# Performance work log

Measured on AMD Instinct MI355X. Metric: run time of the kernel, lower is better.

## Reference

```python
import jax, jax.numpy as jnp
import numpy as np

HIDDEN = 768
HEADS = 12
HEAD_DIM = HIDDEN // HEADS


def setup_inputs() -> dict:
    key = jax.random.key(0)
    ks = jax.random.split(key, 9)
    B, S = 2, 2048
    scale = 1.0 / np.sqrt(HIDDEN)
    return {
        "hidden_states": jax.random.normal(ks[0], (B, S, HIDDEN), jnp.float32),
        "context": jax.random.normal(ks[1], (B, S, HIDDEN), jnp.float32),
        "attention_mask": jnp.zeros((B, 1, 1, S), jnp.float32),
        "Wq": jax.random.normal(ks[2], (HIDDEN, HIDDEN), jnp.float32) * scale,
        "bq": jnp.zeros((HIDDEN,), jnp.float32),
        "Wk": jax.random.normal(ks[3], (HIDDEN, HIDDEN), jnp.float32) * scale,
        "bk": jnp.zeros((HIDDEN,), jnp.float32),
        "Wv": jax.random.normal(ks[4], (HIDDEN, HIDDEN), jnp.float32) * scale,
        "bv": jnp.zeros((HIDDEN,), jnp.float32),
    }


def _split_heads(x):
    # [B, S, H*D] -> [B, H, S, D]
    B, S, _ = x.shape
    return x.reshape(B, S, HEADS, HEAD_DIM).transpose(0, 2, 1, 3)


def reference(hidden_states, context, attention_mask, Wq, bq, Wk, bk, Wv, bv):
    # torch Linear: y = x @ W^T + b
    q = _split_heads(hidden_states @ Wq.T + bq)   # [B,H,Sq,D]
    k = _split_heads(context @ Wk.T + bk)         # [B,H,Sk,D]
    v = _split_heads(context @ Wv.T + bv)         # [B,H,Sk,D]

    scores = jnp.einsum("bhqd,bhkd->bhqk", q, k)
    scores = scores / np.sqrt(HEAD_DIM + 1e-05)
    scores = scores + attention_mask
    probs = jax.nn.softmax(scores, axis=-1)       # dropout p=0 -> identity (eval)
    ctx = jnp.einsum("bhqk,bhkd->bhqd", probs, v) # [B,H,Sq,D]
    B, H, Sq, D = ctx.shape
    return ctx.transpose(0, 2, 1, 3).reshape(B, Sq, H * D)
```

## Files before the change

### kernel.cpp

```cpp
#include <hip/hip_runtime.h>
#include <hip/hip_bf16.h>
#include <math.h>

typedef short s16x8 __attribute__((ext_vector_type(8)));
typedef float f32x4 __attribute__((ext_vector_type(4)));
typedef _Float16 f16x4 __attribute__((ext_vector_type(4)));
typedef __fp16 fp16x2 __attribute__((ext_vector_type(2)));
typedef unsigned short u16;

#define NHEADS 12
#define SEQ 2048
#define NBH 24
#define KDIM 768
#define LOG2E 1.44269504088896f

#define SWZ(row, col) (((row) * 64) + ((col) ^ (((row) & 7) << 3)))
#define SWZ32(row, col) (((row) * 32) + ((col) ^ (((row) & 3) << 3)))

#define GLOAD_LDS16(g, l) __builtin_amdgcn_global_load_lds( \
    (const __attribute__((address_space(1))) unsigned int*)(g), \
    (__attribute__((address_space(3))) unsigned int*)(l), 16, 0, 0)

static __device__ __forceinline__ u16 f2bf(float f) {
    union { float f; unsigned u; } v; v.f = f;
    unsigned r = v.u + 0x7fffu + ((v.u >> 16) & 1u);
    return (u16)(r >> 16);
}
static __device__ __forceinline__ u16 f2h(float f) {
    union { _Float16 h; u16 u; } v; v.h = (_Float16)f;
    return v.u;
}
static __device__ __forceinline__ f16x4 pack4(float a, float b, float c, float d) {
    union { fp16x2 h2[2]; f16x4 h4; } u;
    u.h2[0] = __builtin_amdgcn_cvt_pkrtz(a, b);
    u.h2[1] = __builtin_amdgcn_cvt_pkrtz(c, d);
    return u.h4;
}

__global__ void cvt6_kernel(const float* __restrict__ s0, const float* __restrict__ s1,
                            const float* __restrict__ s2, const float* __restrict__ s3,
                            const float* __restrict__ s4, const float* __restrict__ s5,
                            u16* __restrict__ d0, u16* __restrict__ d1, u16* __restrict__ d2,
                            u16* __restrict__ d3, u16* __restrict__ d4, float* __restrict__ d5,
                            int n4a, int n4w, float qscl) {
    const int z = blockIdx.z;
    int i = blockIdx.x * blockDim.x + threadIdx.x;
    if (z == 5) {
        if (i < (2 * SEQ) / 4) {
            float4 f = ((const float4*)s5)[i];
            f.x *= LOG2E; f.y *= LOG2E; f.z *= LOG2E; f.w *= LOG2E;
            ((float4*)d5)[i] = f;
        }
        return;
    }
    const float* src = (z == 0) ? s0 : (z == 1) ? s1 : (z == 2) ? s2 : (z == 3) ? s3 : s4;
    u16* dst         = (z == 0) ? d0 : (z == 1) ? d1 : (z == 2) ? d2 : (z == 3) ? d3 : d4;
    const int n4     = (z < 2) ? n4a : n4w;
    const float scl  = (z == 2) ? qscl : 1.0f;
    if (i < n4) {
        float4 f = ((const float4*)src)[i];
        ushort4 o;
        o.x = f2bf(f.x * scl); o.y = f2bf(f.y * scl); o.z = f2bf(f.z * scl); o.w = f2bf(f.w * scl);
        ((ushort4*)dst)[i] = o;
    }
}

__launch_bounds__(256)
__global__ void qkv_gemm(const u16* __restrict__ X, const u16* __restrict__ C,
                         const u16* __restrict__ W0, const u16* __restrict__ W1, const u16* __restrict__ W2,
                         const float* __restrict__ b0, const float* __restrict__ b1, const float* __restrict__ b2,
                         u16* __restrict__ Qo, u16* __restrict__ Ko, u16* __restrict__ Vo, float qscl) {
    const int z = blockIdx.z;
    const u16* A    = (z == 0) ? X  : C;
    const u16* W    = (z == 0) ? W0 : (z == 1) ? W1 : W2;
    const float* bi = (z == 0) ? b0 : (z == 1) ? b1 : b2;
    u16* out        = (z == 0) ? Qo : (z == 1) ? Ko : Vo;
    const float bscl = (z == 0) ? qscl : 1.0f;

    __shared__ u16 As[2][128 * 32];
    __shared__ u16 Bs[2][128 * 32];

    const int tid  = threadIdx.x;
    const int lane = tid & 63;
    const int wid  = tid >> 6;
    const int wr = wid >> 1, wc = wid & 1;
    const int l15 = lane & 15, lh = lane >> 4;
    const int mBase = blockIdx.x * 128;
    const int nBase = blockIdx.y * 128;

    size_t aSrc[2], bSrc[2]; int ldsOffG[2];
    #pragma unroll
    for (int i = 0; i < 2; ++i) {
        int L = tid * 8 + i * 2048;
        int row = L >> 5;
        int col = (L & 31) ^ ((row & 3) << 3);
        aSrc[i] = (size_t)(mBase + row) * KDIM + col;
        bSrc[i] = (size_t)(nBase + row) * KDIM + col;
        ldsOffG[i] = wid * 512 + i * 2048;
    }

    f32x4 acc[4][4] = {};

    #pragma unroll
    for (int i = 0; i < 2; ++i) {
        GLOAD_LDS16(&A[aSrc[i]], &As[0][ldsOffG[i]]);
        GLOAD_LDS16(&W[bSrc[i]], &Bs[0][ldsOffG[i]]);
    }

    const int NIT = KDIM / 32;
    for (int it = 0; it < NIT; ++it) {
        const int cur = it & 1;
        __syncthreads();
        if (it + 1 < NIT) {
            const int kb = (it + 1) * 32;
            #pragma unroll
            for (int i = 0; i < 2; ++i) {
                GLOAD_LDS16(&A[aSrc[i] + kb], &As[cur ^ 1][ldsOffG[i]]);
                GLOAD_LDS16(&W[bSrc[i] + kb], &Bs[cur ^ 1][ldsOffG[i]]);
            }
        }
        s16x8 xf[4], wf[4];
        #pragma unroll
        for (int m = 0; m < 4; ++m)
            xf[m] = *(const s16x8*)(&As[cur][SWZ32(wr * 64 + m * 16 + l15, lh * 8)]);
        #pragma unroll
        for (int n = 0; n < 4; ++n)
            wf[n] = *(const s16x8*)(&Bs[cur][SWZ32(wc * 64 + n * 16 + l15, lh * 8)]);
        if (z < 2) {
            #pragma unroll
            for (int m = 0; m < 4; ++m)
                #pragma unroll
                for (int n = 0; n < 4; ++n)
                    acc[m][n] = __builtin_amdgcn_mfma_f32_16x16x32_bf16(wf[n], xf[m], acc[m][n], 0, 0, 0);
        } else {
            #pragma unroll
            for (int m = 0; m < 4; ++m)
                #pragma unroll
                for (int n = 0; n < 4; ++n)
                    acc[m][n] = __builtin_amdgcn_mfma_f32_16x16x32_bf16(xf[m], wf[n], acc[m][n], 0, 0, 0);
        }
    }

    if (z < 2) {
        #pragma unroll
        for (int m = 0; m < 4; ++m) {
            int sg = mBase + wr * 64 + m * 16 + l15;
            int b = sg >> 11, s = sg & 2047;
            #pragma unroll
            for (int n = 0; n < 4; ++n) {
                int d0 = nBase + wc * 64 + n * 16 + lh * 4;
                int h = d0 >> 6, d = d0 & 63;
                float4 bv = *(const float4*)(&bi[d0]);
                ushort4 o;
                o.x = f2bf(acc[m][n][0] + bv.x * bscl);
                o.y = f2bf(acc[m][n][1] + bv.y * bscl);
                o.z = f2bf(acc[m][n][2] + bv.z * bscl);
                o.w = f2bf(acc[m][n][3] + bv.w * bscl);
                *(ushort4*)(&out[(((size_t)(b * NHEADS + h) * SEQ + s) << 6) + d]) = o;
            }
        }
    } else {
        #pragma unroll
        for (int m = 0; m < 4; ++m) {
            #pragma unroll
            for (int n = 0; n < 4; ++n) {
                int colg = nBase + wc * 64 + n * 16 + l15;
                float bv = bi[colg];
                int h = colg >> 6, d = colg & 63;
                int rowg0 = mBase + wr * 64 + m * 16 + lh * 4;
                int b = rowg0 >> 11, s = rowg0 & 2047;
                int sp = (s & ~0x3C) | (((s >> 2) & 3) << 4) | (((s >> 4) & 3) << 2);
                ushort4 o;
                o.x = f2h(acc[m][n][0] + bv);
                o.y = f2h(acc[m][n][1] + bv);
                o.z = f2h(acc[m][n][2] + bv);
                o.w = f2h(acc[m][n][3] + bv);
                *(ushort4*)(&out[(((size_t)(b * NHEADS + h) * 64 + d) << 11) + sp]) = o;
            }
        }
    }
}

template<bool SPLIT>
__launch_bounds__(512)
__global__ void attn_kernel(const u16* __restrict__ Qg, const u16* __restrict__ Kg,
                            const u16* __restrict__ Vg,
                            const float* __restrict__ maskL, float* __restrict__ out,
                            u16* __restrict__ OpartH, float* __restrict__ MLpart) {
    __shared__ u16 Ks[2][64 * 64];
    __shared__ u16 Vt[2][64 * 64];
    __shared__ float maskLds[2048];

    const int tid  = threadIdx.x;
    const int lane = tid & 63;
    const int wid  = tid >> 6;
    const int bh = blockIdx.y;
    const int b = bh / NHEADS;
    const int h = bh % NHEADS;
    const int q0 = blockIdx.x * 128 + wid * 16;
    const int l15 = lane & 15, lh = lane >> 4;
    const int z = SPLIT ? blockIdx.z : 0;
    const int NT = SPLIT ? (SEQ / 128) : (SEQ / 64);
    const int tile0 = z * NT;

    for (int i = tid * 4; i < NT * 64; i += 512 * 4)
        *(float4*)(&maskLds[i]) = *(const float4*)(&maskL[(size_t)b * SEQ + (tile0 << 6) + i]);

    const int srow = tid >> 3;
    const int scol = ((tid & 7) * 8) ^ ((srow & 7) << 3);
    const size_t kSrc = (((size_t)bh * SEQ + srow) << 6) + scol + ((size_t)tile0 << 12);
    const size_t vSrc = (((size_t)bh * 64 + srow) << 11) + scol + (size_t)tile0 * 64;
    const int ldsBase = wid * 512;

    s16x8 qf[2];
    #pragma unroll
    for (int kk = 0; kk < 2; ++kk)
        qf[kk] = *(const s16x8*)(&Qg[(((size_t)bh * SEQ + q0 + l15) << 6) + kk * 32 + lh * 8]);

    f32x4 oacc[4] = {};
    float mrun = -1e30f, lrun = 0.f;

    GLOAD_LDS16(&Kg[kSrc], &Ks[0][ldsBase]);
    GLOAD_LDS16(&Vg[vSrc], &Vt[0][ldsBase]);

    for (int t = 0; t < NT; ++t) {
        const int cur = t & 1;
        __syncthreads();
        if (t + 1 < NT) {
            GLOAD_LDS16(&Kg[kSrc + ((size_t)(t + 1) << 12)], &Ks[cur ^ 1][ldsBase]);
            GLOAD_LDS16(&Vg[vSrc + (size_t)(t + 1) * 64],    &Vt[cur ^ 1][ldsBase]);
        }

        f32x4 sacc[4];
        #pragma unroll
        for (int n = 0; n < 4; ++n) {
            float4 mv = *(const float4*)(&maskLds[t * 64 + n * 16 + lh * 4]);
            sacc[n][0] = mv.x; sacc[n][1] = mv.y; sacc[n][2] = mv.z; sacc[n][3] = mv.w;
        }
        __builtin_amdgcn_s_setprio(1);
        #pragma unroll
        for (int kk = 0; kk < 2; ++kk) {
            #pragma unroll
            for (int n = 0; n < 4; ++n) {
                s16x8 kf = *(const s16x8*)(&Ks[cur][SWZ(n * 16 + l15, kk * 32 + lh * 8)]);
                sacc[n] = __builtin_amdgcn_mfma_f32_16x16x32_bf16(kf, qf[kk], sacc[n], 0, 0, 0);
            }
        }
        __builtin_amdgcn_s_setprio(0);

        float tmax = sacc[0][0];
        #pragma unroll
        for (int n = 0; n < 4; ++n)
            #pragma unroll
            for (int j = 0; j < 4; ++j)
                tmax = fmaxf(tmax, sacc[n][j]);

        if (!__all(tmax - mrun <= 11.0f)) {
            float rmax = fmaxf(tmax, __shfl_xor(tmax, 16));
            rmax = fmaxf(rmax, __shfl_xor(rmax, 32));
            float mnew = fmaxf(mrun, rmax);
            float alpha = __builtin_amdgcn_exp2f(mrun - mnew);
            lrun *= alpha;
            #pragma unroll
            for (int nd = 0; nd < 4; ++nd)
                #pragma unroll
                for (int j = 0; j < 4; ++j)
                    oacc[nd][j] *= alpha;
            mrun = mnew;
        }

        f16x4 pf[4];
        #pragma unroll
        for (int n = 0; n < 4; ++n) {
            float p0 = __builtin_amdgcn_exp2f(sacc[n][0] - mrun);
            float p1 = __builtin_amdgcn_exp2f(sacc[n][1] - mrun);
            float p2 = __builtin_amdgcn_exp2f(sacc[n][2] - mrun);
            float p3 = __builtin_amdgcn_exp2f(sacc[n][3] - mrun);
            lrun += (p0 + p1) + (p2 + p3);
            pf[n] = pack4(p0, p1, p2, p3);
        }

        __builtin_amdgcn_s_setprio(1);
        #pragma unroll
        for (int kk = 0; kk < 2; ++kk) {
            #pragma unroll
            for (int nd = 0; nd < 4; ++nd) {
                s16x8 v2 = *(const s16x8*)(&Vt[cur][SWZ(nd * 16 + l15, lh * 16 + kk * 8)]);
                union { s16x8 s8; f16x4 h4[2]; } u; u.s8 = v2;
                oacc[nd] = __builtin_amdgcn_mfma_f32_16x16x16f16(u.h4[0], pf[2 * kk],     oacc[nd], 0, 0, 0);
                oacc[nd] = __builtin_amdgcn_mfma_f32_16x16x16f16(u.h4[1], pf[2 * kk + 1], oacc[nd], 0, 0, 0);
            }
        }
        __builtin_amdgcn_s_setprio(0);
    }

    lrun += __shfl_xor(lrun, 16);
    lrun += __shfl_xor(lrun, 32);

    const float inv = 1.0f / lrun;
    const int s = q0 + l15;
    if (!SPLIT) {
        #pragma unroll
        for (int nd = 0; nd < 4; ++nd) {
            float4 o;
            o.x = oacc[nd][0] * inv; o.y = oacc[nd][1] * inv;
            o.z = oacc[nd][2] * inv; o.w = oacc[nd][3] * inv;
            *(float4*)(&out[(size_t)(b * SEQ + s) * (NHEADS * 64) + h * 64 + nd * 16 + lh * 4]) = o;
        }
    } else {
        const size_t rbase = ((size_t)(z * NBH + bh) * SEQ + s);
        #pragma unroll
        for (int nd = 0; nd < 4; ++nd) {
            union { f16x4 h4; ushort4 u4; } o;
            o.h4 = pack4(oacc[nd][0] * inv, oacc[nd][1] * inv,
                         oacc[nd][2] * inv, oacc[nd][3] * inv);
            *(ushort4*)(&OpartH[rbase * 64 + nd * 16 + lh * 4]) = o.u4;
        }
        if (lh == 0)
            *(float2*)(&MLpart[rbase * 2]) = make_float2(mrun, lrun);
    }
}

__global__ void combine_kernel(const u16* __restrict__ OpartH, const float* __restrict__ MLpart,
                               float* __restrict__ out) {
    int gid = blockIdx.x * 256 + threadIdx.x;
    int row = gid >> 4, d4 = gid & 15;
    float2 ml0 = ((const float2*)MLpart)[row];
    float2 ml1 = ((const float2*)MLpart)[NBH * SEQ + row];
    float m = fmaxf(ml0.x, ml1.x);
    float w0 = __builtin_amdgcn_exp2f(ml0.x - m) * ml0.y;
    float w1 = __builtin_amdgcn_exp2f(ml1.x - m) * ml1.y;
    float inv = 1.0f / (w0 + w1);
    w0 *= inv; w1 *= inv;
    union { ushort4 u4; f16x4 h4; } a, c;
    a.u4 = *(const ushort4*)(&OpartH[(size_t)row * 64 + d4 * 4]);
    c.u4 = *(const ushort4*)(&OpartH[(size_t)NBH * SEQ * 64 + (size_t)row * 64 + d4 * 4]);
    float4 o;
    o.x = (float)a.h4[0] * w0 + (float)c.h4[0] * w1;
    o.y = (float)a.h4[1] * w0 + (float)c.h4[1] * w1;
    o.z = (float)a.h4[2] * w0 + (float)c.h4[2] * w1;
    o.w = (float)a.h4[3] * w0 + (float)c.h4[3] * w1;
    int bh = row >> 11, s = row & 2047;
    int b = bh / NHEADS, hh = bh % NHEADS;
    *(float4*)(&out[(size_t)(b * SEQ + s) * (NHEADS * 64) + hh * 64 + d4 * 4]) = o;
}

extern "C" void kernel_launch(void* const* d_in, const int* in_sizes, int n_in,
                              void* d_out, int out_size, void* d_ws, size_t ws_size,
                              hipStream_t stream) {
    const float* hidden  = (const float*)d_in[0];
    const float* context = (const float*)d_in[1];
    const float* mask    = (const float*)d_in[2];
    const float* Wq = (const float*)d_in[3];
    const float* bq = (const float*)d_in[4];
    const float* Wk = (const float*)d_in[5];
    const float* bk = (const float*)d_in[6];
    const float* Wv = (const float*)d_in[7];
    const float* bv = (const float*)d_in[8];
    float* out = (float*)d_out;

    char* ws = (char*)d_ws;
    const size_t XSZ = (size_t)4096 * 768 * 2;
    const size_t WSZ = (size_t)768 * 768 * 2;
    u16* X16  = (u16*)(ws);
    u16* C16  = (u16*)(ws + XSZ);
    u16* W16q = (u16*)(ws + 2 * XSZ);
    u16* W16k = (u16*)(ws + 2 * XSZ + WSZ);
    u16* W16v = (u16*)(ws + 2 * XSZ + 2 * WSZ);
    u16* Q16  = (u16*)(ws + 2 * XSZ + 3 * WSZ);
    u16* K16  = (u16*)(ws + 3 * XSZ + 3 * WSZ);
    u16* V16  = (u16*)(ws + 4 * XSZ + 3 * WSZ);
    const size_t MASKL_OFF = 5 * XSZ + 3 * WSZ;
    float* maskL = (float*)(ws + MASKL_OFF);
    const size_t OPART_OFF = MASKL_OFF + 2 * SEQ * sizeof(float) + 256;
    u16* OpartH = (u16*)(ws + OPART_OFF);
    const size_t ML_OFF = OPART_OFF + (size_t)2 * NBH * SEQ * 64 * 2;
    float* MLpart = (float*)(ws + ML_OFF);
    const size_t WS_NEED_SPLIT = ML_OFF + (size_t)2 * NBH * SEQ * 2 * 4;

    const float qscl = (float)((1.0 / sqrt(64.0 + 1e-5)) * 1.44269504088896);

    const int n4x = 4096 * 768 / 4;
    const int n4w = 768 * 768 / 4;
    cvt6_kernel<<<dim3((n4x + 255) / 256, 1, 6), 256, 0, stream>>>(
        hidden, context, Wq, Wk, Wv, mask,
        X16, C16, W16q, W16k, W16v, maskL, n4x, n4w, qscl);

    qkv_gemm<<<dim3(4096 / 128, 768 / 128, 3), 256, 0, stream>>>(
        X16, C16, W16q, W16k, W16v, bq, bk, bv, Q16, K16, V16, qscl);

    if (ws_size >= WS_NEED_SPLIT) {
        attn_kernel<true><<<dim3(SEQ / 128, NBH, 2), 512, 0, stream>>>(
            Q16, K16, V16, maskL, out, OpartH, MLpart);
        combine_kernel<<<(NBH * SEQ * 16) / 256, 256, 0, stream>>>(OpartH, MLpart, out);
    } else {
        attn_kernel<false><<<dim3(SEQ / 128, NBH, 1), 512, 0, stream>>>(
            Q16, K16, V16, maskL, out, OpartH, MLpart);
    }
}
```

Baseline: 101.4 us.

## Triple-buffer QKV GEMM LDS with vmcnt waits and a pair-row swizzle

Moves the QKV projection GEMM from double to triple LDS buffering with a prefetch distance of two k-steps. A fine-grained s_waitcnt vmcnt plus a raw s_barrier replaces __syncthreads, and prefetches are issued after the MFMAs instead of before. It also changes the LDS layout so two 32-wide rows share one 64-wide row under the 8-way XOR swizzle, meant to reduce bank conflicts on fragment reads. The cost is 50% more LDS per block, which may lower occupancy, and it relies on hand-counted vmcnt values staying correct.

```diff
diff --git a/kernel.cpp b/kernel.cpp
--- a/kernel.cpp
+++ b/kernel.cpp
@@ -15,7 +15,6 @@
 #define LOG2E 1.44269504088896f
 
 #define SWZ(row, col) (((row) * 64) + ((col) ^ (((row) & 7) << 3)))
-#define SWZ32(row, col) (((row) * 32) + ((col) ^ (((row) & 3) << 3)))
 
 #define GLOAD_LDS16(g, l) __builtin_amdgcn_global_load_lds( \
     (const __attribute__((address_space(1))) unsigned int*)(g), \
@@ -77,8 +76,8 @@
     u16* out        = (z == 0) ? Qo : (z == 1) ? Ko : Vo;
     const float bscl = (z == 0) ? qscl : 1.0f;
 
-    __shared__ u16 As[2][128 * 32];
-    __shared__ u16 Bs[2][128 * 32];
+    __shared__ u16 As[3][4096];
+    __shared__ u16 Bs[3][4096];
 
     const int tid  = threadIdx.x;
     const int lane = tid & 63;
@@ -88,44 +87,51 @@
     const int mBase = blockIdx.x * 128;
     const int nBase = blockIdx.y * 128;
 
-    size_t aSrc[2], bSrc[2]; int ldsOffG[2];
+    size_t aSrc[2], bSrc[2]; int ldsOff[2];
     #pragma unroll
     for (int i = 0; i < 2; ++i) {
-        int L = tid * 8 + i * 2048;
-        int row = L >> 5;
-        int col = (L & 31) ^ ((row & 3) << 3);
+        int L = i * 2048 + tid * 8;
+        int prow = L >> 6;
+        int pcol = (L & 63) ^ ((prow & 7) << 3);
+        int row = (prow << 1) | (pcol >> 5);
+        int col = pcol & 31;
         aSrc[i] = (size_t)(mBase + row) * KDIM + col;
         bSrc[i] = (size_t)(nBase + row) * KDIM + col;
-        ldsOffG[i] = wid * 512 + i * 2048;
-    }
+        ldsOff[i] = i * 2048 + wid * 512;
+    }
+
+#define G_STAGE(step, buf) do { \
+        const size_t kb_ = (size_t)(step) * 32; \
+        GLOAD_LDS16(&A[aSrc[0] + kb_], &As[buf][ldsOff[0]]); \
+        GLOAD_LDS16(&A[aSrc[1] + kb_], &As[buf][ldsOff[1]]); \
+        GLOAD_LDS16(&W[bSrc[0] + kb_], &Bs[buf][ldsOff[0]]); \
+        GLOAD_LDS16(&W[bSrc[1] + kb_], &Bs[buf][ldsOff[1]]); \
+    } while (0)
 
     f32x4 acc[4][4] = {};
 
-    #pragma unroll
-    for (int i = 0; i < 2; ++i) {
-        GLOAD_LDS16(&A[aSrc[i]], &As[0][ldsOffG[i]]);
-        GLOAD_LDS16(&W[bSrc[i]], &Bs[0][ldsOffG[i]]);
-    }
+    G_STAGE(0, 0);
+    G_STAGE(1, 1);
 
     const int NIT = KDIM / 32;
+    int cur = 0;
     for (int it = 0; it < NIT; ++it) {
-        const int cur = it & 1;
-        __syncthreads();
-        if (it + 1 < NIT) {
-            const int kb = (it + 1) * 32;
-            #pragma unroll
-            for (int i = 0; i < 2; ++i) {
-                GLOAD_LDS16(&A[aSrc[i] + kb], &As[cur ^ 1][ldsOffG[i]]);
-                GLOAD_LDS16(&W[bSrc[i] + kb], &Bs[cur ^ 1][ldsOffG[i]]);
-            }
-        }
+        if (it + 1 < NIT) asm volatile("s_waitcnt vmcnt(4)" ::: "memory");
+        else              asm volatile("s_waitcnt vmcnt(0)" ::: "memory");
+        __builtin_amdgcn_s_barrier();
+        __builtin_amdgcn_sched_barrier(0);
+
         s16x8 xf[4], wf[4];
         #pragma unroll
-        for (int m = 0; m < 4; ++m)
-            xf[m] = *(const s16x8*)(&As[cur][SWZ32(wr * 64 + m * 16 + l15, lh * 8)]);
-        #pragma unroll
-        for (int n = 0; n < 4; ++n)
-            wf[n] = *(const s16x8*)(&Bs[cur][SWZ32(wc * 64 + n * 16 + l15, lh * 8)]);
+        for (int m = 0; m < 4; ++m) {
+            int row = wr * 64 + m * 16 + l15;
+            xf[m] = *(const s16x8*)(&As[cur][SWZ(row >> 1, (row & 1) * 32 + lh * 8)]);
+        }
+        #pragma unroll
+        for (int n = 0; n < 4; ++n) {
+            int row = wc * 64 + n * 16 + l15;
+            wf[n] = *(const s16x8*)(&Bs[cur][SWZ(row >> 1, (row & 1) * 32 + lh * 8)]);
+        }
         if (z < 2) {
             #pragma unroll
             for (int m = 0; m < 4; ++m)
@@ -139,7 +145,14 @@
                 for (int n = 0; n < 4; ++n)
                     acc[m][n] = __builtin_amdgcn_mfma_f32_16x16x32_bf16(xf[m], wf[n], acc[m][n], 0, 0, 0);
         }
-    }
+
+        if (it + 2 < NIT) {
+            int nxt = cur + 2; if (nxt >= 3) nxt -= 3;
+            G_STAGE(it + 2, nxt);
+        }
+        ++cur; if (cur == 3) cur = 0;
+    }
+#undef G_STAGE
 
     if (z < 2) {
         #pragma unroll
```

After: 93.41 us. 1.09x faster.
